# Kernel tuning notes

Hardware: AMD Instinct MI355X
Metric: run time of the kernel (lower is better)

## Reference

```python
import jax, jax.numpy as jnp
import numpy as np

# DilationSumLayer with kernel_size=(7,7), padding='same' (pad=3 per side).
# The torch module's unfold (dense L @ x @ R matmuls) + kron(ones, weight) add
# + MaxPool2d(7, stride=7) is exactly grayscale morphological dilation:
#   out[..., i, j] = max_{a,b} ( xpad[..., i+a, j+b] + w[a, b] )
KH, KW = 7, 7
PAD = 3  # kernel_size // 2, 'same' padding, zero-padded (F.pad default)


def setup_inputs() -> dict:
    key = jax.random.key(0)
    k1, k2 = jax.random.split(key)
    x = jax.random.normal(k1, (8, 8, 512, 512), dtype=jnp.float32)      # (B, C, H, W)
    weight = jax.random.normal(k2, (KH, KW), dtype=jnp.float32)          # structuring element
    return {"x": x, "weight": weight}


def reference(x, weight):
    kh, kw = KH, KW
    xp = jnp.pad(x, ((0, 0), (0, 0), (PAD, PAD), (PAD, PAD)))  # (B, C, H+2p, W+2p)
    Ho = xp.shape[-2] - kh + 1  # == H ('same')
    Wo = xp.shape[-1] - kw + 1  # == W
    # Running max over the 49 fixed kernel offsets (small static loop; each
    # iteration is a fused shifted-view add + elementwise max, no big stack).
    out = jnp.full(x.shape[:-2] + (Ho, Wo), -jnp.inf, dtype=x.dtype)
    for a in range(kh):
        for b in range(kw):
            out = jnp.maximum(out, xp[..., a:a + Ho, b:b + Wo] + weight[a, b])
    return out
```

## Files before the change

kernel.cpp:

```cpp
#include <hip/hip_runtime.h>


#define HH 512
#define WW 512

typedef float v2f __attribute__((ext_vector_type(2)));

__device__ __align__(16) const float ZROW[272] = {};

__device__ __forceinline__ float max3f(float a, float b, float c) {
  float d;
  asm("v_max3_f32 %0, %1, %2, %3" : "=v"(d) : "v"(a), "v"(b), "v"(c));
  return d;
}

#define LOADROW(E, K)                                                        \
  {                                                                          \
    const int r_ = row0 - 3 + (K);                               \
    const float* rb_ = ((unsigned)r_ < (unsigned)HH)                         \
                           ? (xp + (ptrdiff_t)r_ * WW)                       \
                           : zrb;                         \
    const float* p0_ = okL ? rb_ + col0 - 4 : &ZROW[0];                      \
    const float* p2_ = okR ? rb_ + col0 + 4 : &ZROW[0];                      \
    float4 v0_ = *reinterpret_cast<const float4*>(p0_);                      \
    float4 v1_ = *reinterpret_cast<const float4*>(rb_ + col0);               \
    float4 v2_ = *reinterpret_cast<const float4*>(p2_);                      \
    E[0] = (v2f){v0_.x, v0_.y};  E[1] = (v2f){v0_.z, v0_.w};                 \
    E[2] = (v2f){v1_.x, v1_.y};  E[3] = (v2f){v1_.z, v1_.w};                 \
    E[4] = (v2f){v2_.x, v2_.y};  E[5] = (v2f){v2_.z, v2_.w};                 \
  }

#define ONEOUT(T, K, J, P1, P2, P3, S)                                       \
  {                                                                          \
    const int a_ = (K) - (T);                                                \
    const v2f c01_ = (P1) + w2[a_][0];                     \
    const v2f c23_ = (P2) + w2[a_][1];                                       \
    const v2f c45_ = (P3) + w2[a_][2];                                       \
    const float c6_ = (S) + w6[a_];                                          \
    const float t1_ = max3f(c01_.x, c01_.y, c23_.x);                         \
    const float t2_ = max3f(c23_.y, c45_.x, c45_.y);                         \
    acc[T][J] = ((K) == (T))                                                 \
                    ? max3f(t1_, t2_, c6_)                  \
                    : max3f(t1_, t2_, fmaxf(c6_, acc[T][J]));                \
  }

#define COMPROW(E, K)                                                        \
  {                                                                          \
    const v2f o0_ = (v2f){E[0].y, E[1].x};                                   \
    const v2f o1_ = (v2f){E[1].y, E[2].x};                                   \
    const v2f o2_ = (v2f){E[2].y, E[3].x};                                   \
    const v2f o3_ = (v2f){E[3].y, E[4].x};                                   \
    _Pragma("unroll") for (int t = 0; t < 8; ++t) {                          \
      if (t <= (K) && t + 6 >= (K)) {                                        \
        ONEOUT(t, K, 0, o0_, o1_, o2_, E[3].y);                              \
        ONEOUT(t, K, 1, E[1], E[2], E[3], E[4].x);                           \
        ONEOUT(t, K, 2, o1_, o2_, o3_, E[4].y);                              \
        ONEOUT(t, K, 3, E[2], E[3], E[4], E[5].x);                           \
      }                                                                      \
    }                                                                        \
  }

#define STOREROW(T)                                                          \
  {                                                                          \
    float* orow_ = op + (ptrdiff_t)(row0 + (T)) * WW + col0;                 \
    *reinterpret_cast<float4*>(orow_) =                                      \
        make_float4(acc[T][0], acc[T][1], acc[T][2], acc[T][3]);             \
  }

__global__ __launch_bounds__(256) void dilate7(const float* __restrict__ x,
                                               const float* __restrict__ wg,
                                               float* __restrict__ out) {
  const int tid = threadIdx.x;
  const int lc = tid & 63;
  const int colbase = blockIdx.x * 256;
  const int col0 = colbase + lc * 4;
  const int row0 =
      __builtin_amdgcn_readfirstlane(blockIdx.y * 32 + (tid >> 6) * 8);

  const size_t plane_off = (size_t)blockIdx.z * (size_t)(HH * WW);
  const float* xp = x + plane_off;
  float* op = out + plane_off;

  float wv[49];
#pragma unroll
  for (int i = 0; i < 49; ++i)
    wv[i] = __int_as_float(__builtin_amdgcn_readfirstlane(__float_as_int(wg[i])));
  v2f w2[7][3];
  float w6[7];
#pragma unroll
  for (int a = 0; a < 7; ++a) {
    w2[a][0] = (v2f){wv[7 * a + 0], wv[7 * a + 1]};
    w2[a][1] = (v2f){wv[7 * a + 2], wv[7 * a + 3]};
    w2[a][2] = (v2f){wv[7 * a + 4], wv[7 * a + 5]};
    w6[a] = wv[7 * a + 6];
  }

  const float* zrb = ZROW + 4 - colbase;
  const bool okL = (col0 >= 4);
  const bool okR = (col0 + 8 <= WW);

  float acc[8][4];
  v2f eA[6], eB[6];

  LOADROW(eA, 0);
  LOADROW(eB, 1);   COMPROW(eA, 0);
  LOADROW(eA, 2);   COMPROW(eB, 1);
  LOADROW(eB, 3);   COMPROW(eA, 2);
  LOADROW(eA, 4);   COMPROW(eB, 3);
  LOADROW(eB, 5);   COMPROW(eA, 4);
  LOADROW(eA, 6);   COMPROW(eB, 5);
  LOADROW(eB, 7);   COMPROW(eA, 6);   STOREROW(0);
  LOADROW(eA, 8);   COMPROW(eB, 7);   STOREROW(1);
  LOADROW(eB, 9);   COMPROW(eA, 8);   STOREROW(2);
  LOADROW(eA, 10);  COMPROW(eB, 9);   STOREROW(3);
  LOADROW(eB, 11);  COMPROW(eA, 10);  STOREROW(4);
  LOADROW(eA, 12);  COMPROW(eB, 11);  STOREROW(5);
  LOADROW(eB, 13);  COMPROW(eA, 12);  STOREROW(6);
  COMPROW(eB, 13);  STOREROW(7);
}

extern "C" void kernel_launch(void* const* d_in, const int* in_sizes, int n_in,
                              void* d_out, int out_size, void* d_ws, size_t ws_size,
                              hipStream_t stream) {
  const float* x = (const float*)d_in[0];
  const float* w = (const float*)d_in[1];
  float* out = (float*)d_out;
  const int planes = in_sizes[0] / (HH * WW);
  dim3 grid(2, 16, planes);
  dilate7<<<grid, dim3(256, 1, 1), 0, stream>>>(x, w, out);
}
```

Before: 41.81 us.

## Stage input rows in an LDS ring buffer with register-prefetched bands

Each block now covers 64 rows instead of 32. It first stages a 22-row halo tile into a 38-row LDS ring buffer. It then processes four 16-row bands, where each wave computes 4 output rows from LDS. While a band is being computed, the rows needed by the next band are prefetched from global memory into registers and written into the free ring slots before a barrier. The aim is to cut the redundant per-thread global halo row reads and overlap global loads with compute. The cost is extra LDS traffic, barriers, and fewer blocks in the grid.

```diff
diff --git a/kernel.cpp b/kernel.cpp
--- a/kernel.cpp
+++ b/kernel.cpp
@@ -6,29 +6,13 @@
 
 typedef float v2f __attribute__((ext_vector_type(2)));
 
-__device__ __align__(16) const float ZROW[272] = {};
+__device__ __align__(16) const float ZP4[4] = {0.f, 0.f, 0.f, 0.f};
 
 __device__ __forceinline__ float max3f(float a, float b, float c) {
   float d;
   asm("v_max3_f32 %0, %1, %2, %3" : "=v"(d) : "v"(a), "v"(b), "v"(c));
   return d;
 }
-
-#define LOADROW(E, K)                                                        \
-  {                                                                          \
-    const int r_ = row0 - 3 + (K);                               \
-    const float* rb_ = ((unsigned)r_ < (unsigned)HH)                         \
-                           ? (xp + (ptrdiff_t)r_ * WW)                       \
-                           : zrb;                         \
-    const float* p0_ = okL ? rb_ + col0 - 4 : &ZROW[0];                      \
-    const float* p2_ = okR ? rb_ + col0 + 4 : &ZROW[0];                      \
-    float4 v0_ = *reinterpret_cast<const float4*>(p0_);                      \
-    float4 v1_ = *reinterpret_cast<const float4*>(rb_ + col0);               \
-    float4 v2_ = *reinterpret_cast<const float4*>(p2_);                      \
-    E[0] = (v2f){v0_.x, v0_.y};  E[1] = (v2f){v0_.z, v0_.w};                 \
-    E[2] = (v2f){v1_.x, v1_.y};  E[3] = (v2f){v1_.z, v1_.w};                 \
-    E[4] = (v2f){v2_.x, v2_.y};  E[5] = (v2f){v2_.z, v2_.w};                 \
-  }
 
 #define ONEOUT(T, K, J, P1, P2, P3, S)                                       \
   {                                                                          \
@@ -50,7 +34,7 @@
     const v2f o1_ = (v2f){E[1].y, E[2].x};                                   \
     const v2f o2_ = (v2f){E[2].y, E[3].x};                                   \
     const v2f o3_ = (v2f){E[3].y, E[4].x};                                   \
-    _Pragma("unroll") for (int t = 0; t < 8; ++t) {                          \
+    _Pragma("unroll") for (int t = 0; t < 4; ++t) {                          \
       if (t <= (K) && t + 6 >= (K)) {                                        \
         ONEOUT(t, K, 0, o0_, o1_, o2_, E[3].y);                              \
         ONEOUT(t, K, 1, E[1], E[2], E[3], E[4].x);                           \
@@ -60,9 +44,22 @@
     }                                                                        \
   }
 
-#define STOREROW(T)                                                          \
+#define LOADDS(E, K)                                                         \
   {                                                                          \
-    float* orow_ = op + (ptrdiff_t)(row0 + (T)) * WW + col0;                 \
+    int o_ = bando + tr4 + (K);                                              \
+    o_ -= (o_ >= 38) ? 38 : 0;                                               \
+    const float* lr_ = ldsf + o_ * 264 + lc4;                                \
+    float4 v0_ = *reinterpret_cast<const float4*>(lr_);                      \
+    float4 v1_ = *reinterpret_cast<const float4*>(lr_ + 4);                  \
+    float4 v2_ = *reinterpret_cast<const float4*>(lr_ + 8);                  \
+    E[0] = (v2f){v0_.x, v0_.y};  E[1] = (v2f){v0_.z, v0_.w};                 \
+    E[2] = (v2f){v1_.x, v1_.y};  E[3] = (v2f){v1_.z, v1_.w};                 \
+    E[4] = (v2f){v2_.x, v2_.y};  E[5] = (v2f){v2_.z, v2_.w};                 \
+  }
+
+#define STOREROW4(T)                                                         \
+  {                                                                          \
+    float* orow_ = op + (ptrdiff_t)(rowband + tr4 + (T)) * WW + col0;        \
     *reinterpret_cast<float4*>(orow_) =                                      \
         make_float4(acc[T][0], acc[T][1], acc[T][2], acc[T][3]);             \
   }
@@ -70,12 +67,15 @@
 __global__ __launch_bounds__(256) void dilate7(const float* __restrict__ x,
                                                const float* __restrict__ wg,
                                                float* __restrict__ out) {
+  __shared__ float ldsf[38 * 264];
+
   const int tid = threadIdx.x;
   const int lc = tid & 63;
+  const int lc4 = lc << 2;
   const int colbase = blockIdx.x * 256;
-  const int col0 = colbase + lc * 4;
-  const int row0 =
-      __builtin_amdgcn_readfirstlane(blockIdx.y * 32 + (tid >> 6) * 8);
+  const int col0 = colbase + lc4;
+  const int tr4 = __builtin_amdgcn_readfirstlane((tid >> 6) << 2);
+  const int row0blk = blockIdx.y * 64;
 
   const size_t plane_off = (size_t)blockIdx.z * (size_t)(HH * WW);
   const float* xp = x + plane_off;
@@ -95,28 +95,77 @@
     w6[a] = wv[7 * a + 6];
   }
 
-  const float* zrb = ZROW + 4 - colbase;
-  const bool okL = (col0 >= 4);
-  const bool okR = (col0 + 8 <= WW);
+  {
+    unsigned r_ = __umulhi((unsigned)tid, 0x7C1F07C4u) >> 5;
+    int c_ = tid - (int)r_ * 66;
+#pragma unroll
+    for (int i = 0; i < 6; ++i) {
+      int q = i * 256 + tid;
+      if (q < 1452) {
+        int g = row0blk - 3 + (int)r_;
+        int gc = colbase - 4 + (c_ << 2);
+        bool ok = ((unsigned)g < (unsigned)HH) && ((unsigned)gc < (unsigned)WW);
+        const float* src = ok ? (xp + (ptrdiff_t)g * WW + gc) : &ZP4[0];
+        float4 v = *reinterpret_cast<const float4*>(src);
+        *reinterpret_cast<float4*>(ldsf + (int)r_ * 264 + (c_ << 2)) = v;
+      }
+      r_ += 3; c_ += 58; if (c_ >= 66) { c_ -= 66; ++r_; }
+    }
+  }
+  __syncthreads();
 
-  float acc[8][4];
-  v2f eA[6], eB[6];
+  float acc[4][4];
+  v2f rvA[6], rvB[6];
 
-  LOADROW(eA, 0);
-  LOADROW(eB, 1);   COMPROW(eA, 0);
-  LOADROW(eA, 2);   COMPROW(eB, 1);
-  LOADROW(eB, 3);   COMPROW(eA, 2);
-  LOADROW(eA, 4);   COMPROW(eB, 3);
-  LOADROW(eB, 5);   COMPROW(eA, 4);
-  LOADROW(eA, 6);   COMPROW(eB, 5);
-  LOADROW(eB, 7);   COMPROW(eA, 6);   STOREROW(0);
-  LOADROW(eA, 8);   COMPROW(eB, 7);   STOREROW(1);
-  LOADROW(eB, 9);   COMPROW(eA, 8);   STOREROW(2);
-  LOADROW(eA, 10);  COMPROW(eB, 9);   STOREROW(3);
-  LOADROW(eB, 11);  COMPROW(eA, 10);  STOREROW(4);
-  LOADROW(eA, 12);  COMPROW(eB, 11);  STOREROW(5);
-  LOADROW(eB, 13);  COMPROW(eA, 12);  STOREROW(6);
-  COMPROW(eB, 13);  STOREROW(7);
+#pragma unroll 1
+  for (int b = 0; b < 4; ++b) {
+    const int bando = 16 * b;
+    const int rowband = row0blk + bando;
+
+    float4 sv[5];
+    if (b < 3) {
+      unsigned r_ = __umulhi((unsigned)tid, 0x7C1F07C4u) >> 5;
+      int c_ = tid - (int)r_ * 66;
+      const int grb = row0blk + bando + 19;
+#pragma unroll
+      for (int i = 0; i < 5; ++i) {
+        if (i < 4 || tid < 32) {
+          int g = grb + (int)r_;
+          int gc = colbase - 4 + (c_ << 2);
+          bool ok = ((unsigned)g < (unsigned)HH) && ((unsigned)gc < (unsigned)WW);
+          const float* src = ok ? (xp + (ptrdiff_t)g * WW + gc) : &ZP4[0];
+          sv[i] = *reinterpret_cast<const float4*>(src);
+        }
+        r_ += 3; c_ += 58; if (c_ >= 66) { c_ -= 66; ++r_; }
+      }
+    }
+
+    LOADDS(rvA, 0);
+    LOADDS(rvB, 1);  COMPROW(rvA, 0);
+    LOADDS(rvA, 2);  COMPROW(rvB, 1);
+    LOADDS(rvB, 3);  COMPROW(rvA, 2);
+    LOADDS(rvA, 4);  COMPROW(rvB, 3);
+    LOADDS(rvB, 5);  COMPROW(rvA, 4);
+    LOADDS(rvA, 6);  COMPROW(rvB, 5);
+    LOADDS(rvB, 7);  COMPROW(rvA, 6);  STOREROW4(0);
+    LOADDS(rvA, 8);  COMPROW(rvB, 7);  STOREROW4(1);
+    LOADDS(rvB, 9);  COMPROW(rvA, 8);  STOREROW4(2);
+                     COMPROW(rvB, 9);  STOREROW4(3);
+
+    if (b < 3) {
+      unsigned r_ = __umulhi((unsigned)tid, 0x7C1F07C4u) >> 5;
+      int c_ = tid - (int)r_ * 66;
+      int sb = bando + 22; sb -= (sb >= 38) ? 38 : 0;
+#pragma unroll
+      for (int i = 0; i < 5; ++i) {
+        if (i < 4 || tid < 32) {
+          *reinterpret_cast<float4*>(ldsf + (sb + (int)r_) * 264 + (c_ << 2)) = sv[i];
+        }
+        r_ += 3; c_ += 58; if (c_ >= 66) { c_ -= 66; ++r_; }
+      }
+      __syncthreads();
+    }
+  }
 }
 
 extern "C" void kernel_launch(void* const* d_in, const int* in_sizes, int n_in,
@@ -126,6 +175,6 @@
   const float* w = (const float*)d_in[1];
   float* out = (float*)d_out;
   const int planes = in_sizes[0] / (HH * WW);
-  dim3 grid(2, 16, planes);
+  dim3 grid(2, 8, planes);
   dilate7<<<grid, dim3(256, 1, 1), 0, stream>>>(x, w, out);
 }
```

Result: slower. 49.42 us (+18.2%).

## Widen per-thread tile to 8 columns by 8 rows to cut halo loads

Applied to the files above, without the earlier changes.

Each thread now computes an 8x8 output tile instead of 4x8, loading four float4 per input row instead of three, so the horizontal halo costs a smaller share of each row load. Blocks are rearranged as 32 column-threads by 8 row-groups, and the grid halves in y. Row bounds are now checked per load pointer rather than through an offset zero-row trick, which shrinks the zero buffer. The cost is higher register pressure (64 accumulators plus 16 input pairs) and half as many blocks, which may lower occupancy and latency hiding.

```diff
diff --git a/kernel.cpp b/kernel.cpp
--- a/kernel.cpp
+++ b/kernel.cpp
@@ -6,7 +6,7 @@
 
 typedef float v2f __attribute__((ext_vector_type(2)));
 
-__device__ __align__(16) const float ZROW[272] = {};
+__device__ __align__(16) const float ZROW[16] = {};
 
 __device__ __forceinline__ float max3f(float a, float b, float c) {
   float d;
@@ -16,18 +16,21 @@
 
 #define LOADROW(E, K)                                                        \
   {                                                                          \
-    const int r_ = row0 - 3 + (K);                               \
-    const float* rb_ = ((unsigned)r_ < (unsigned)HH)                         \
-                           ? (xp + (ptrdiff_t)r_ * WW)                       \
-                           : zrb;                         \
-    const float* p0_ = okL ? rb_ + col0 - 4 : &ZROW[0];                      \
-    const float* p2_ = okR ? rb_ + col0 + 4 : &ZROW[0];                      \
+    const int r_ = row0 - 3 + (K);                                           \
+    const bool rok_ = ((unsigned)r_ < (unsigned)HH);                         \
+    const float* rp_ = xp + (ptrdiff_t)r_ * WW + (col0 - 4);                 \
+    const float* p0_ = (rok_ && okL) ? rp_ : zp;                             \
+    const float* p1_ = rok_ ? rp_ + 4 : zp;                                  \
+    const float* p2_ = rok_ ? rp_ + 8 : zp;                                  \
+    const float* p3_ = (rok_ && okR) ? rp_ + 12 : zp;                        \
     float4 v0_ = *reinterpret_cast<const float4*>(p0_);                      \
-    float4 v1_ = *reinterpret_cast<const float4*>(rb_ + col0);               \
+    float4 v1_ = *reinterpret_cast<const float4*>(p1_);                      \
     float4 v2_ = *reinterpret_cast<const float4*>(p2_);                      \
+    float4 v3_ = *reinterpret_cast<const float4*>(p3_);                      \
     E[0] = (v2f){v0_.x, v0_.y};  E[1] = (v2f){v0_.z, v0_.w};                 \
     E[2] = (v2f){v1_.x, v1_.y};  E[3] = (v2f){v1_.z, v1_.w};                 \
     E[4] = (v2f){v2_.x, v2_.y};  E[5] = (v2f){v2_.z, v2_.w};                 \
+    E[6] = (v2f){v3_.x, v3_.y};  E[7] = (v2f){v3_.z, v3_.w};                 \
   }
 
 #define ONEOUT(T, K, J, P1, P2, P3, S)                                       \
@@ -50,12 +53,18 @@
     const v2f o1_ = (v2f){E[1].y, E[2].x};                                   \
     const v2f o2_ = (v2f){E[2].y, E[3].x};                                   \
     const v2f o3_ = (v2f){E[3].y, E[4].x};                                   \
+    const v2f o4_ = (v2f){E[4].y, E[5].x};                                   \
+    const v2f o5_ = (v2f){E[5].y, E[6].x};                                   \
     _Pragma("unroll") for (int t = 0; t < 8; ++t) {                          \
-      if (t <= (K) && t + 6 >= (K)) {                                        \
+      if (t <= (K) && t + 6 >= (K)) {            \
         ONEOUT(t, K, 0, o0_, o1_, o2_, E[3].y);                              \
         ONEOUT(t, K, 1, E[1], E[2], E[3], E[4].x);                           \
         ONEOUT(t, K, 2, o1_, o2_, o3_, E[4].y);                              \
         ONEOUT(t, K, 3, E[2], E[3], E[4], E[5].x);                           \
+        ONEOUT(t, K, 4, o2_, o3_, o4_, E[5].y);                              \
+        ONEOUT(t, K, 5, E[3], E[4], E[5], E[6].x);                           \
+        ONEOUT(t, K, 6, o3_, o4_, o5_, E[6].y);                              \
+        ONEOUT(t, K, 7, E[4], E[5], E[6], E[7].x);                           \
       }                                                                      \
     }                                                                        \
   }
@@ -65,17 +74,18 @@
     float* orow_ = op + (ptrdiff_t)(row0 + (T)) * WW + col0;                 \
     *reinterpret_cast<float4*>(orow_) =                                      \
         make_float4(acc[T][0], acc[T][1], acc[T][2], acc[T][3]);             \
+    *reinterpret_cast<float4*>(orow_ + 4) =                                  \
+        make_float4(acc[T][4], acc[T][5], acc[T][6], acc[T][7]);             \
   }
 
 __global__ __launch_bounds__(256) void dilate7(const float* __restrict__ x,
                                                const float* __restrict__ wg,
                                                float* __restrict__ out) {
   const int tid = threadIdx.x;
-  const int lc = tid & 63;
-  const int colbase = blockIdx.x * 256;
-  const int col0 = colbase + lc * 4;
-  const int row0 =
-      __builtin_amdgcn_readfirstlane(blockIdx.y * 32 + (tid >> 6) * 8);
+  const int lc = tid & 31;
+  const int tr = tid >> 5;
+  const int col0 = blockIdx.x * 256 + lc * 8;
+  const int row0 = blockIdx.y * 64 + tr * 8;
 
   const size_t plane_off = (size_t)blockIdx.z * (size_t)(HH * WW);
   const float* xp = x + plane_off;
@@ -95,12 +105,12 @@
     w6[a] = wv[7 * a + 6];
   }
 
-  const float* zrb = ZROW + 4 - colbase;
+  const float* zp = &ZROW[0];
   const bool okL = (col0 >= 4);
-  const bool okR = (col0 + 8 <= WW);
+  const bool okR = (col0 + 16 <= WW);
 
-  float acc[8][4];
-  v2f eA[6], eB[6];
+  float acc[8][8];
+  v2f eA[8], eB[8];
 
   LOADROW(eA, 0);
   LOADROW(eB, 1);   COMPROW(eA, 0);
@@ -126,6 +136,6 @@
   const float* w = (const float*)d_in[1];
   float* out = (float*)d_out;
   const int planes = in_sizes[0] / (HH * WW);
-  dim3 grid(2, 16, planes);
+  dim3 grid(2, 8, planes);
   dilate7<<<grid, dim3(256, 1, 1), 0, stream>>>(x, w, out);
 }
```

Measured after the change: 43.22 us. +3.4%, slower.
